# Kernel optimization log

Hardware: AMD Instinct MI355X
Metric: run time of the kernel (lower is better)

## Reference

```python
import jax, jax.numpy as jnp
import numpy as np

N = 50000      # nodes
E = 800000     # edges (avg degree 16)
F_IN = 64      # node_feature_space
H = 64         # hidden_dim
G = 16         # graphs in batch
BN_EPS = 1e-5


def setup_inputs() -> dict:
    key = jax.random.key(0)
    ks = jax.random.split(key, 8)
    x = jax.random.normal(ks[0], (N, F_IN), jnp.float32)
    edge_index = jax.random.randint(ks[1], (2, E), 0, N, dtype=jnp.int64)
    batch = jnp.sort(jax.random.randint(ks[2], (N,), 0, G, dtype=jnp.int64))
    init = lambda k, shp, fan: jax.random.normal(k, shp, jnp.float32) / np.float32(np.sqrt(fan))
    params = dict(
        W1_0=init(ks[3], (F_IN, H), F_IN), b1_0=jnp.zeros((H,), jnp.float32),
        W2_0=init(ks[4], (H, H), H),       b2_0=jnp.zeros((H,), jnp.float32),
        g_0=jnp.ones((H,), jnp.float32),   be_0=jnp.zeros((H,), jnp.float32),
        W1_1=init(ks[5], (H, H), H),       b1_1=jnp.zeros((H,), jnp.float32),
        W2_1=init(ks[6], (H, H), H),       b2_1=jnp.zeros((H,), jnp.float32),
        g_1=jnp.ones((H,), jnp.float32),   be_1=jnp.zeros((H,), jnp.float32),
    )
    return dict(x=x, edge_index=edge_index, batch=batch, **params)


def _gin_layer(x, src, dst, W1, b1, W2, b2, g, be):
    # GINConv (eps=0): h_i = MLP(x_i + sum_{j->i} x_j)
    agg = jax.ops.segment_sum(x[src], dst, num_segments=N)   # [N, d]
    h = x + agg
    h = jnp.maximum(h @ W1 + b1, 0.0) @ W2 + b2              # Linear-ReLU-Linear
    # BatchNorm1d (training-mode batch stats, biased variance as in torch)
    mu = h.mean(axis=0)
    var = h.var(axis=0)
    h = (h - mu) * jax.lax.rsqrt(var + BN_EPS) * g + be
    return jnp.maximum(h, 0.0)                               # ReLU


def reference(x, edge_index, batch,
              W1_0, b1_0, W2_0, b2_0, g_0, be_0,
              W1_1, b1_1, W2_1, b2_1, g_1, be_1):
    src, dst = edge_index[0], edge_index[1]
    x = _gin_layer(x, src, dst, W1_0, b1_0, W2_0, b2_0, g_0, be_0)
    x = _gin_layer(x, src, dst, W1_1, b1_1, W2_1, b2_1, g_1, be_1)
    # global_mean_pool over graph ids
    cnt = jax.ops.segment_sum(jnp.ones((N,), x.dtype), batch, num_segments=G)
    sums = jax.ops.segment_sum(x, batch, num_segments=G)
    h_graph = sums / jnp.maximum(cnt, 1.0)[:, None]
    return (x, h_graph)
```

## Files before the change

kernel.cpp:

```cpp
#include <hip/hip_runtime.h>
#include <hip/hip_bf16.h>


constexpr int NN = 50000;
constexpr int NE = 800000;
constexpr int HD = 64;
constexpr int NG = 16;
constexpr float BN_EPS = 1e-5f;
constexpr int SCAN_BLOCKS = (NN + 255) / 256;

__global__ __launch_bounds__(256)
void count_kernel(const int* __restrict__ ei, int* __restrict__ cnt) {
    int e = blockIdx.x * 256 + threadIdx.x;
    if (e >= NE) return;
    atomicAdd(&cnt[ei[NE + e]], 1);
}

__global__ __launch_bounds__(256)
void scan1_kernel(const int* __restrict__ cnt, int* __restrict__ row_ptr,
                  int* __restrict__ partials) {
    int i = blockIdx.x * 256 + threadIdx.x;
    int v = (i < NN) ? cnt[i] : 0;
    __shared__ int s[256];
    s[threadIdx.x] = v;
    __syncthreads();
#pragma unroll
    for (int off = 1; off < 256; off <<= 1) {
        int add = (threadIdx.x >= off) ? s[threadIdx.x - off] : 0;
        __syncthreads();
        s[threadIdx.x] += add;
        __syncthreads();
    }
    if (i < NN) row_ptr[i] = s[threadIdx.x] - v;
    if (threadIdx.x == 255) partials[blockIdx.x] = s[255];
}

__global__ __launch_bounds__(256)
void scan2_kernel(int* __restrict__ partials, int* __restrict__ poffs) {
    int v = (threadIdx.x < SCAN_BLOCKS) ? partials[threadIdx.x] : 0;
    __shared__ int s[256];
    s[threadIdx.x] = v;
    __syncthreads();
#pragma unroll
    for (int off = 1; off < 256; off <<= 1) {
        int add = (threadIdx.x >= off) ? s[threadIdx.x - off] : 0;
        __syncthreads();
        s[threadIdx.x] += add;
        __syncthreads();
    }
    poffs[threadIdx.x] = s[threadIdx.x] - v;
}

__global__ __launch_bounds__(256)
void scan3_kernel(int* __restrict__ row_ptr, const int* __restrict__ poffs,
                  int* __restrict__ cursor) {
    int i = blockIdx.x * 256 + threadIdx.x;
    if (i < NN) {
        int v = row_ptr[i] + poffs[blockIdx.x];
        row_ptr[i] = v;
        cursor[i] = v;
    }
    if (i == 0) row_ptr[NN] = NE;
}

__global__ __launch_bounds__(256)
void place_kernel(const int* __restrict__ ei, int* __restrict__ cursor,
                  int* __restrict__ csr) {
    int e = blockIdx.x * 256 + threadIdx.x;
    if (e >= NE) return;
    int pos = atomicAdd(&cursor[ei[NE + e]], 1);
    csr[pos] = ei[e];
}

__global__ __launch_bounds__(256)
void x2bf_kernel(const float* __restrict__ x, __hip_bfloat16* __restrict__ xb,
                 int* __restrict__ cnt) {
    int i4 = blockIdx.x * 256 + threadIdx.x;
    if (i4 < NN) cnt[i4] = 0;
    if (i4 >= NN * HD / 4) return;
    float4 v = *(const float4*)(x + (size_t)i4 * 4);
    union { ushort4 u; __hip_bfloat16 b[4]; } p;
    p.b[0] = __float2bfloat16(v.x);
    p.b[1] = __float2bfloat16(v.y);
    p.b[2] = __float2bfloat16(v.z);
    p.b[3] = __float2bfloat16(v.w);
    *(ushort4*)((unsigned short*)xb + (size_t)i4 * 4) = p.u;
}

__global__ __launch_bounds__(256)
void agg_kernel(const float* __restrict__ x, const __hip_bfloat16* __restrict__ xb,
                const int* __restrict__ row_ptr, const int* __restrict__ csr,
                float* __restrict__ h, float* __restrict__ stats) {
    if (blockIdx.x == 0 && threadIdx.x < 128) stats[threadIdx.x] = 0.f;
    int row = blockIdx.x * 4 + (threadIdx.x >> 6);
    int lane = threadIdx.x & 63;
    int s = row_ptr[row], e = row_ptr[row + 1];
    int cnt = e - s;
    int ids = (lane < cnt) ? csr[s + lane] : 0;
    float acc = x[(size_t)row * HD + lane];
    int m = min(cnt, 64);
    int j = 0;
    float a0 = 0.f, a1 = 0.f, a2 = 0.f, a3 = 0.f;
    for (; j + 4 <= m; j += 4) {
        int nb0 = __shfl(ids, j);
        int nb1 = __shfl(ids, j + 1);
        int nb2 = __shfl(ids, j + 2);
        int nb3 = __shfl(ids, j + 3);
        float v0 = __bfloat162float(xb[(size_t)nb0 * HD + lane]);
        float v1 = __bfloat162float(xb[(size_t)nb1 * HD + lane]);
        float v2 = __bfloat162float(xb[(size_t)nb2 * HD + lane]);
        float v3 = __bfloat162float(xb[(size_t)nb3 * HD + lane]);
        a0 += v0; a1 += v1; a2 += v2; a3 += v3;
    }
    acc += (a0 + a1) + (a2 + a3);
    for (; j < m; j++) {
        int nb = __shfl(ids, j);
        acc += __bfloat162float(xb[(size_t)nb * HD + lane]);
    }
    for (int jj = s + 64; jj < e; jj++) {
        acc += __bfloat162float(xb[(size_t)csr[jj] * HD + lane]);
    }
    h[(size_t)row * HD + lane] = acc;
}

__global__ __launch_bounds__(256)
void mlp_kernel(const float* __restrict__ hin, float* __restrict__ hout,
                const float* __restrict__ W1, const float* __restrict__ b1,
                const float* __restrict__ W2, const float* __restrict__ b2,
                float* __restrict__ stats, float* __restrict__ psums) {
    __shared__ float sh[128 * 65];
    __shared__ float sW[64 * 64];
    __shared__ float sb[64];
    __shared__ float red[2][4][64];
    int tid = threadIdx.x;
    int base = blockIdx.x * 128;

    if (blockIdx.x == 0) {
        float4 z = make_float4(0.f, 0.f, 0.f, 0.f);
        *(float4*)(psums + tid * 4) = z;
    }
    for (int i = tid; i < 4096; i += 256) sW[i] = W1[i];
    if (tid < 64) sb[tid] = b1[tid];
#pragma unroll
    for (int i = 0; i < 8; i++) {
        int i4 = tid + 256 * i;
        int row = i4 >> 4, col = (i4 & 15) * 4;
        int grow = base + row;
        float4 v = (grow < NN) ? *(const float4*)(hin + (size_t)grow * HD + col)
                               : make_float4(0.f, 0.f, 0.f, 0.f);
        float* d = sh + row * 65 + col;
        d[0] = v.x; d[1] = v.y; d[2] = v.z; d[3] = v.w;
    }
    __syncthreads();

    int wv = tid >> 6;
    int lane = tid & 63;

    float acc0[16], acc1[16];
#pragma unroll
    for (int j = 0; j < 16; j++) { acc0[j] = sb[wv * 16 + j]; acc1[j] = acc0[j]; }
    for (int k = 0; k < 64; k++) {
        float a0 = sh[lane * 65 + k];
        float a1 = sh[(64 + lane) * 65 + k];
        const float4* wr = (const float4*)(sW + k * 64 + wv * 16);
#pragma unroll
        for (int q = 0; q < 4; q++) {
            float4 w = wr[q];
            acc0[4 * q + 0] = fmaf(a0, w.x, acc0[4 * q + 0]);
            acc0[4 * q + 1] = fmaf(a0, w.y, acc0[4 * q + 1]);
            acc0[4 * q + 2] = fmaf(a0, w.z, acc0[4 * q + 2]);
            acc0[4 * q + 3] = fmaf(a0, w.w, acc0[4 * q + 3]);
            acc1[4 * q + 0] = fmaf(a1, w.x, acc1[4 * q + 0]);
            acc1[4 * q + 1] = fmaf(a1, w.y, acc1[4 * q + 1]);
            acc1[4 * q + 2] = fmaf(a1, w.z, acc1[4 * q + 2]);
            acc1[4 * q + 3] = fmaf(a1, w.w, acc1[4 * q + 3]);
        }
    }
    __syncthreads();

#pragma unroll
    for (int j = 0; j < 16; j++) {
        sh[lane * 65 + wv * 16 + j] = fmaxf(acc0[j], 0.f);
        sh[(64 + lane) * 65 + wv * 16 + j] = fmaxf(acc1[j], 0.f);
    }
    for (int i = tid; i < 4096; i += 256) sW[i] = W2[i];
    if (tid < 64) sb[tid] = b2[tid];
    __syncthreads();

#pragma unroll
    for (int j = 0; j < 16; j++) { acc0[j] = sb[wv * 16 + j]; acc1[j] = acc0[j]; }
    for (int k = 0; k < 64; k++) {
        float a0 = sh[lane * 65 + k];
        float a1 = sh[(64 + lane) * 65 + k];
        const float4* wr = (const float4*)(sW + k * 64 + wv * 16);
#pragma unroll
        for (int q = 0; q < 4; q++) {
            float4 w = wr[q];
            acc0[4 * q + 0] = fmaf(a0, w.x, acc0[4 * q + 0]);
            acc0[4 * q + 1] = fmaf(a0, w.y, acc0[4 * q + 1]);
            acc0[4 * q + 2] = fmaf(a0, w.z, acc0[4 * q + 2]);
            acc0[4 * q + 3] = fmaf(a0, w.w, acc0[4 * q + 3]);
            acc1[4 * q + 0] = fmaf(a1, w.x, acc1[4 * q + 0]);
            acc1[4 * q + 1] = fmaf(a1, w.y, acc1[4 * q + 1]);
            acc1[4 * q + 2] = fmaf(a1, w.z, acc1[4 * q + 2]);
            acc1[4 * q + 3] = fmaf(a1, w.w, acc1[4 * q + 3]);
        }
    }
    __syncthreads();
#pragma unroll
    for (int j = 0; j < 16; j++) {
        sh[lane * 65 + wv * 16 + j] = acc0[j];
        sh[(64 + lane) * 65 + wv * 16 + j] = acc1[j];
    }
    __syncthreads();

#pragma unroll
    for (int i = 0; i < 8; i++) {
        int i4 = tid + 256 * i;
        int row = i4 >> 4, col = (i4 & 15) * 4;
        int grow = base + row;
        if (grow < NN) {
            const float* s = sh + row * 65 + col;
            *(float4*)(hout + (size_t)grow * HD + col) =
                make_float4(s[0], s[1], s[2], s[3]);
        }
    }

    {
        int col = tid & 63;
        int r0 = (tid >> 6) * 32;
        float s = 0.f, ss = 0.f;
#pragma unroll
        for (int r = 0; r < 32; r++) {
            float v = (base + r0 + r < NN) ? sh[(r0 + r) * 65 + col] : 0.f;
            s += v;
            ss += v * v;
        }
        red[0][tid >> 6][col] = s;
        red[1][tid >> 6][col] = ss;
        __syncthreads();
        if (tid < 64) {
            float S = red[0][0][col] + red[0][1][col] + red[0][2][col] + red[0][3][col];
            atomicAdd(stats + col, S);
        } else if (tid < 128) {
            float SS = red[1][0][col] + red[1][1][col] + red[1][2][col] + red[1][3][col];
            atomicAdd(stats + 64 + col, SS);
        }
    }
}

__global__ __launch_bounds__(256)
void norm_kernel(float* h, const float* __restrict__ stats,
                 const float* __restrict__ g, const float* __restrict__ be,
                 __hip_bfloat16* __restrict__ xb) {
    size_t i4 = (size_t)blockIdx.x * 256 + threadIdx.x;
    if (i4 >= (size_t)NN * HD / 4) return;
    size_t off = i4 * 4;
    int col = (int)(off & 63);
    float4 v = *(const float4*)(h + off);
    float4 sm = *(const float4*)(stats + col);
    float4 sq = *(const float4*)(stats + 64 + col);
    float4 gg = *(const float4*)(g + col);
    float4 bb = *(const float4*)(be + col);
    const float inv = 1.f / (float)NN;
    float4 o;
    {
        float mu = sm.x * inv, var = sq.x * inv - mu * mu;
        float sc = gg.x * rsqrtf(var + BN_EPS);
        o.x = fmaxf((v.x - mu) * sc + bb.x, 0.f);
    }
    {
        float mu = sm.y * inv, var = sq.y * inv - mu * mu;
        float sc = gg.y * rsqrtf(var + BN_EPS);
        o.y = fmaxf((v.y - mu) * sc + bb.y, 0.f);
    }
    {
        float mu = sm.z * inv, var = sq.z * inv - mu * mu;
        float sc = gg.z * rsqrtf(var + BN_EPS);
        o.z = fmaxf((v.z - mu) * sc + bb.z, 0.f);
    }
    {
        float mu = sm.w * inv, var = sq.w * inv - mu * mu;
        float sc = gg.w * rsqrtf(var + BN_EPS);
        o.w = fmaxf((v.w - mu) * sc + bb.w, 0.f);
    }
    *(float4*)(h + off) = o;
    union { ushort4 u; __hip_bfloat16 b[4]; } p;
    p.b[0] = __float2bfloat16(o.x);
    p.b[1] = __float2bfloat16(o.y);
    p.b[2] = __float2bfloat16(o.z);
    p.b[3] = __float2bfloat16(o.w);
    *(ushort4*)((unsigned short*)xb + off) = p.u;
}

__global__ __launch_bounds__(256)
void pool_partial_kernel(const float* __restrict__ x, const int* __restrict__ batch,
                         float* __restrict__ sums) {
    int col = threadIdx.x & 63;
    int rl = threadIdx.x >> 6;
    int rs = blockIdx.x * 250;
    int re = rs + 250;
    int cur = -1;
    float acc = 0.f;
    for (int r = rs + rl; r < re; r += 4) {
        int g = batch[r];
        float v = x[(size_t)r * HD + col];
        if (g != cur) {
            if (cur >= 0) atomicAdd(&sums[cur * HD + col], acc);
            cur = g;
            acc = v;
        } else {
            acc += v;
        }
    }
    if (cur >= 0) atomicAdd(&sums[cur * HD + col], acc);
}

__device__ __forceinline__ int lower_bound_batch(const int* __restrict__ b, int val) {
    int lo = 0, hi = NN;
    while (lo < hi) {
        int mid = (lo + hi) >> 1;
        if (b[mid] < val) lo = mid + 1;
        else hi = mid;
    }
    return lo;
}

__global__ __launch_bounds__(1024)
void pool_finalize_kernel(const float* __restrict__ sums, const int* __restrict__ batch,
                          float* __restrict__ out) {
    int g = threadIdx.x >> 6;
    int col = threadIdx.x & 63;
    int s = lower_bound_batch(batch, g);
    int e = lower_bound_batch(batch, g + 1);
    float cnt = (float)(e - s);
    out[g * HD + col] = sums[g * HD + col] / fmaxf(cnt, 1.f);
}

extern "C" void kernel_launch(void* const* d_in, const int* in_sizes, int n_in,
                              void* d_out, int out_size, void* d_ws, size_t ws_size,
                              hipStream_t stream) {
    const float* x = (const float*)d_in[0];
    const int* ei = (const int*)d_in[1];
    const int* batch = (const int*)d_in[2];
    const float* W1_0 = (const float*)d_in[3];
    const float* b1_0 = (const float*)d_in[4];
    const float* W2_0 = (const float*)d_in[5];
    const float* b2_0 = (const float*)d_in[6];
    const float* g_0 = (const float*)d_in[7];
    const float* be_0 = (const float*)d_in[8];
    const float* W1_1 = (const float*)d_in[9];
    const float* b1_1 = (const float*)d_in[10];
    const float* W2_1 = (const float*)d_in[11];
    const float* b2_1 = (const float*)d_in[12];
    const float* g_1 = (const float*)d_in[13];
    const float* be_1 = (const float*)d_in[14];

    float* out = (float*)d_out;

    float* buf_h = (float*)d_ws;
    float* stats = buf_h + (size_t)NN * HD;
    float* psums = stats + 128;
    int* row_ptr = (int*)(psums + 1024);
    int* cnt = row_ptr + (NN + 2);
    int* partials = cnt + NN;
    int* poffs = partials + 256;
    int* csr = poffs + 256;
    __hip_bfloat16* xb = (__hip_bfloat16*)(csr + NE);

    dim3 b256(256);
    int egrid = (NE + 255) / 256;
    int mlp_grid = (NN + 127) / 128;
    int norm_grid = (NN * HD / 4 + 255) / 256;
    int agg_grid = NN / 4;

    x2bf_kernel<<<norm_grid, b256, 0, stream>>>(x, xb, cnt);
    count_kernel<<<egrid, b256, 0, stream>>>(ei, cnt);
    scan1_kernel<<<SCAN_BLOCKS, b256, 0, stream>>>(cnt, row_ptr, partials);
    scan2_kernel<<<1, b256, 0, stream>>>(partials, poffs);
    scan3_kernel<<<SCAN_BLOCKS, b256, 0, stream>>>(row_ptr, poffs, cnt);
    place_kernel<<<egrid, b256, 0, stream>>>(ei, cnt, csr);

    agg_kernel<<<agg_grid, b256, 0, stream>>>(x, xb, row_ptr, csr, buf_h, stats);
    mlp_kernel<<<mlp_grid, b256, 0, stream>>>(buf_h, out, W1_0, b1_0, W2_0, b2_0, stats, psums);
    norm_kernel<<<norm_grid, b256, 0, stream>>>(out, stats, g_0, be_0, xb);

    agg_kernel<<<agg_grid, b256, 0, stream>>>(out, xb, row_ptr, csr, buf_h, stats);
    mlp_kernel<<<mlp_grid, b256, 0, stream>>>(buf_h, out, W1_1, b1_1, W2_1, b2_1, stats, psums);
    norm_kernel<<<norm_grid, b256, 0, stream>>>(out, stats, g_1, be_1, xb);

    pool_partial_kernel<<<200, b256, 0, stream>>>(out, batch, psums);
    pool_finalize_kernel<<<1, dim3(1024), 0, stream>>>(psums, batch, out + (size_t)NN * HD);
}
```

Baseline: 330.7 us.

## Split neighbor aggregation into two column-half passes with half-wave rows

```diff
diff --git a/kernel.cpp b/kernel.cpp
--- a/kernel.cpp
+++ b/kernel.cpp
@@ -88,39 +88,60 @@
 }
 
 __global__ __launch_bounds__(256)
-void agg_kernel(const float* __restrict__ x, const __hip_bfloat16* __restrict__ xb,
-                const int* __restrict__ row_ptr, const int* __restrict__ csr,
-                float* __restrict__ h, float* __restrict__ stats) {
+void agg_half_kernel(const float* __restrict__ x, const __hip_bfloat16* __restrict__ xb,
+                     const int* __restrict__ row_ptr, const int* __restrict__ csr,
+                     float* __restrict__ h, float* __restrict__ stats, int pass) {
     if (blockIdx.x == 0 && threadIdx.x < 128) stats[threadIdx.x] = 0.f;
-    int row = blockIdx.x * 4 + (threadIdx.x >> 6);
-    int lane = threadIdx.x & 63;
+    int tid = threadIdx.x;
+    int lane = tid & 63;
+    int i31 = lane & 31;
+    int hb = lane & 32;
+    int row = blockIdx.x * 8 + (tid >> 6) * 2 + (lane >> 5);
+    int col = pass * 32 + i31;
     int s = row_ptr[row], e = row_ptr[row + 1];
     int cnt = e - s;
-    int ids = (lane < cnt) ? csr[s + lane] : 0;
-    float acc = x[(size_t)row * HD + lane];
-    int m = min(cnt, 64);
+    int ids = (i31 < cnt) ? csr[s + i31] : 0;
+    float acc = x[(size_t)row * HD + col];
+    int m = min(cnt, 32);
     int j = 0;
     float a0 = 0.f, a1 = 0.f, a2 = 0.f, a3 = 0.f;
-    for (; j + 4 <= m; j += 4) {
-        int nb0 = __shfl(ids, j);
-        int nb1 = __shfl(ids, j + 1);
-        int nb2 = __shfl(ids, j + 2);
-        int nb3 = __shfl(ids, j + 3);
-        float v0 = __bfloat162float(xb[(size_t)nb0 * HD + lane]);
-        float v1 = __bfloat162float(xb[(size_t)nb1 * HD + lane]);
-        float v2 = __bfloat162float(xb[(size_t)nb2 * HD + lane]);
-        float v3 = __bfloat162float(xb[(size_t)nb3 * HD + lane]);
+    float a4 = 0.f, a5 = 0.f, a6 = 0.f, a7 = 0.f;
+    for (; j + 8 <= m; j += 8) {
+        int nb0 = __shfl(ids, hb + j);
+        int nb1 = __shfl(ids, hb + j + 1);
+        int nb2 = __shfl(ids, hb + j + 2);
+        int nb3 = __shfl(ids, hb + j + 3);
+        int nb4 = __shfl(ids, hb + j + 4);
+        int nb5 = __shfl(ids, hb + j + 5);
+        int nb6 = __shfl(ids, hb + j + 6);
+        int nb7 = __shfl(ids, hb + j + 7);
+        float v0 = __bfloat162float(xb[(size_t)nb0 * HD + col]);
+        float v1 = __bfloat162float(xb[(size_t)nb1 * HD + col]);
+        float v2 = __bfloat162float(xb[(size_t)nb2 * HD + col]);
+        float v3 = __bfloat162float(xb[(size_t)nb3 * HD + col]);
+        float v4 = __bfloat162float(xb[(size_t)nb4 * HD + col]);
+        float v5 = __bfloat162float(xb[(size_t)nb5 * HD + col]);
+        float v6 = __bfloat162float(xb[(size_t)nb6 * HD + col]);
+        float v7 = __bfloat162float(xb[(size_t)nb7 * HD + col]);
         a0 += v0; a1 += v1; a2 += v2; a3 += v3;
-    }
-    acc += (a0 + a1) + (a2 + a3);
+        a4 += v4; a5 += v5; a6 += v6; a7 += v7;
+    }
+    acc += ((a0 + a1) + (a2 + a3)) + ((a4 + a5) + (a6 + a7));
     for (; j < m; j++) {
-        int nb = __shfl(ids, j);
-        acc += __bfloat162float(xb[(size_t)nb * HD + lane]);
-    }
-    for (int jj = s + 64; jj < e; jj++) {
-        acc += __bfloat162float(xb[(size_t)csr[jj] * HD + lane]);
-    }
-    h[(size_t)row * HD + lane] = acc;
+        int nb = __shfl(ids, hb + j);
+        acc += __bfloat162float(xb[(size_t)nb * HD + col]);
+    }
+    if (cnt > 32) {
+        int ids2 = (32 + i31 < cnt) ? csr[s + 32 + i31] : 0;
+        int m2 = min(cnt, 64);
+        for (j = 32; j < m2; j++) {
+            int nb = __shfl(ids2, hb + (j - 32));
+            acc += __bfloat162float(xb[(size_t)nb * HD + col]);
+        }
+        for (j = 64; j < cnt; j++)
+            acc += __bfloat162float(xb[(size_t)csr[s + j] * HD + col]);
+    }
+    h[(size_t)row * HD + col] = acc;
 }
 
 __global__ __launch_bounds__(256)
@@ -372,7 +393,7 @@
     int egrid = (NE + 255) / 256;
     int mlp_grid = (NN + 127) / 128;
     int norm_grid = (NN * HD / 4 + 255) / 256;
-    int agg_grid = NN / 4;
+    int aggh_grid = NN / 8;
 
     x2bf_kernel<<<norm_grid, b256, 0, stream>>>(x, xb, cnt);
     count_kernel<<<egrid, b256, 0, stream>>>(ei, cnt);
@@ -381,11 +402,13 @@
     scan3_kernel<<<SCAN_BLOCKS, b256, 0, stream>>>(row_ptr, poffs, cnt);
     place_kernel<<<egrid, b256, 0, stream>>>(ei, cnt, csr);
 
-    agg_kernel<<<agg_grid, b256, 0, stream>>>(x, xb, row_ptr, csr, buf_h, stats);
+    agg_half_kernel<<<aggh_grid, b256, 0, stream>>>(x, xb, row_ptr, csr, buf_h, stats, 0);
+    agg_half_kernel<<<aggh_grid, b256, 0, stream>>>(x, xb, row_ptr, csr, buf_h, stats, 1);
     mlp_kernel<<<mlp_grid, b256, 0, stream>>>(buf_h, out, W1_0, b1_0, W2_0, b2_0, stats, psums);
     norm_kernel<<<norm_grid, b256, 0, stream>>>(out, stats, g_0, be_0, xb);
 
-    agg_kernel<<<agg_grid, b256, 0, stream>>>(out, xb, row_ptr, csr, buf_h, stats);
+    agg_half_kernel<<<aggh_grid, b256, 0, stream>>>(out, xb, row_ptr, csr, buf_h, stats, 0);
+    agg_half_kernel<<<aggh_grid, b256, 0, stream>>>(out, xb, row_ptr, csr, buf_h, stats, 1);
     mlp_kernel<<<mlp_grid, b256, 0, stream>>>(buf_h, out, W1_1, b1_1, W2_1, b2_1, stats, psums);
     norm_kernel<<<norm_grid, b256, 0, stream>>>(out, stats, g_1, be_1, xb);
 
```

Result: slower. 359.4 us (+8.7%).
